# Kernel tuning notes

Measured on AMD Instinct MI355X. Metric: run time of the kernel, lower is better.

The kernel has to match this reference:

```python
import jax, jax.numpy as jnp
import numpy as np

EMB = 768
HEADS = 12
HEAD_DIM = EMB // HEADS
FF = 4 * EMB
EPS = 1e-5


def setup_inputs() -> dict:
    key = jax.random.key(0)
    ks = jax.random.split(key, 12)
    s = 0.02
    return {
        "x": jax.random.normal(ks[0], (4, 2048, EMB), dtype=jnp.float32),
        "ln1_scale": jnp.ones((EMB,), jnp.float32),
        "ln1_shift": jnp.zeros((EMB,), jnp.float32),
        # weights stored [in, out] (transpose of torch Linear layout)
        "wq": jax.random.normal(ks[1], (EMB, EMB), jnp.float32) * s,
        "wk": jax.random.normal(ks[2], (EMB, EMB), jnp.float32) * s,
        "wv": jax.random.normal(ks[3], (EMB, EMB), jnp.float32) * s,
        "wo": jax.random.normal(ks[4], (EMB, EMB), jnp.float32) * s,
        "bo": jnp.zeros((EMB,), jnp.float32),
        "ln2_scale": jnp.ones((EMB,), jnp.float32),
        "ln2_shift": jnp.zeros((EMB,), jnp.float32),
        "w1": jax.random.normal(ks[5], (EMB, FF), jnp.float32) * s,
        "b1": jnp.zeros((FF,), jnp.float32),
        "w2": jax.random.normal(ks[6], (FF, EMB), jnp.float32) * s,
        "b2": jnp.zeros((EMB,), jnp.float32),
    }


def _layernorm(x, scale, shift):
    mean = jnp.mean(x, axis=-1, keepdims=True)
    var = jnp.mean(jnp.square(x - mean), axis=-1, keepdims=True)  # unbiased=False
    return scale * (x - mean) / jnp.sqrt(var + EPS) + shift


def _gelu_tanh(x):
    c = jnp.sqrt(jnp.float32(2.0 / np.pi))
    return 0.5 * x * (1.0 + jnp.tanh(c * (x + 0.044715 * x * x * x)))


def _attention(x, wq, wk, wv, wo, bo):
    b, s, _ = x.shape
    q = (x @ wq).reshape(b, s, HEADS, HEAD_DIM).transpose(0, 2, 1, 3)
    k = (x @ wk).reshape(b, s, HEADS, HEAD_DIM).transpose(0, 2, 1, 3)
    v = (x @ wv).reshape(b, s, HEADS, HEAD_DIM).transpose(0, 2, 1, 3)
    scores = jnp.einsum("bhqd,bhkd->bhqk", q, k)  # [B,H,S,S]
    causal = jnp.tril(jnp.ones((s, s), dtype=bool))
    scores = jnp.where(causal, scores, -jnp.inf)
    weights = jax.nn.softmax(scores / jnp.sqrt(jnp.float32(HEAD_DIM)), axis=-1)
    ctx = jnp.einsum("bhqk,bhkd->bhqd", weights, v)
    ctx = ctx.transpose(0, 2, 1, 3).reshape(b, s, EMB)
    return ctx @ wo + bo


def reference(x, ln1_scale, ln1_shift, wq, wk, wv, wo, bo,
              ln2_scale, ln2_shift, w1, b1, w2, b2):
    # dropout rate is 0.0 (inference) -> identity
    x = x + _attention(_layernorm(x, ln1_scale, ln1_shift), wq, wk, wv, wo, bo)
    h = _layernorm(x, ln2_scale, ln2_shift)
    h = _gelu_tanh(h @ w1 + b1) @ w2 + b2
    return x + h
```

## Files before the change

kernel.cpp:

```cpp
#include <hip/hip_runtime.h>
#include <stdint.h>

#define EMB 768
#define SEQ 2048
#define BATCH 4
#define NHEADS 12
#define HDIM 64
#define FFDIM 3072
#define NTOK (BATCH*SEQ)
#define LNEPS 1e-5f
#define QSCALE 0.1803368801111137f

typedef __attribute__((ext_vector_type(8))) short bf16x8;
typedef __attribute__((ext_vector_type(4))) float f32x4;

__device__ __forceinline__ uint16_t f2bf(float f){
  union { float f; uint32_t u; } v; v.f = f;
  uint32_t r = v.u + 0x7fffu + ((v.u >> 16) & 1u);
  return (uint16_t)(r >> 16);
}
__device__ __forceinline__ uint32_t pk_rhu(float lo, float hi){
  union { float f; uint32_t u; } a, b; a.f = lo; b.f = hi;
  return __builtin_amdgcn_perm(b.u + 0x8000u, a.u + 0x8000u, 0x07060302u);
}

typedef __attribute__((address_space(3))) uint32_t lds32_t;
typedef __attribute__((address_space(1))) const uint32_t glb32_t;
__device__ __forceinline__ void gload16(const void* g, void* l){
  __builtin_amdgcn_global_load_lds((glb32_t*)(uintptr_t)g,
                                   (lds32_t*)(uintptr_t)l, 16, 0, 0);
}

struct TPtrs { const float* src[6]; uint16_t* dst[6]; };
__global__ __launch_bounds__(256) void transpose_all(TPtrs tp){
  int idx = blockIdx.x;
  int which, bx, by, K, N;
  if (idx < 2304){ which = idx/576; int l = idx - which*576; bx = l%24; by = l/24; K = 768;  N = 768;  }
  else if (idx < 4608){ which = 4; int l = idx-2304; bx = l%96; by = l/96; K = 768;  N = 3072; }
  else { which = 5; int l = idx-4608; bx = l%24; by = l/24; K = 3072; N = 768;  }
  const float* w = tp.src[which];
  uint16_t* wt   = tp.dst[which];
  __shared__ uint16_t tile[32][33];
  int n0 = bx*32, k0 = by*32;
  #pragma unroll
  for (int i=0;i<4;i++){
    int k = threadIdx.y + i*8;
    tile[k][threadIdx.x] = f2bf(w[(size_t)(k0+k)*N + n0 + threadIdx.x]);
  }
  __syncthreads();
  #pragma unroll
  for (int i=0;i<4;i++){
    int n = threadIdx.y + i*8;
    wt[(size_t)(n0+n)*K + k0 + threadIdx.x] = tile[threadIdx.x][n];
  }
}

__global__ __launch_bounds__(256) void ln_kernel(const float* __restrict__ x,
    const float* __restrict__ sc, const float* __restrict__ sh,
    uint16_t* __restrict__ out)
{
  int row = blockIdx.x*4 + (threadIdx.x>>6);
  int ln = threadIdx.x & 63;
  const float4* xr = (const float4*)(x + (size_t)row*EMB);
  float4 v0 = xr[ln], v1 = xr[64+ln], v2 = xr[128+ln];
  float s  = v0.x+v0.y+v0.z+v0.w + v1.x+v1.y+v1.z+v1.w + v2.x+v2.y+v2.z+v2.w;
  float s2 = v0.x*v0.x+v0.y*v0.y+v0.z*v0.z+v0.w*v0.w
           + v1.x*v1.x+v1.y*v1.y+v1.z*v1.z+v1.w*v1.w
           + v2.x*v2.x+v2.y*v2.y+v2.z*v2.z+v2.w*v2.w;
  #pragma unroll
  for (int off=1;off<64;off<<=1){ s += __shfl_xor(s,off); s2 += __shfl_xor(s2,off); }
  float mean = s*(1.f/768.f);
  float var  = s2*(1.f/768.f) - mean*mean;
  float rstd = rsqrtf(var + LNEPS);
  uint16_t* orow = out + (size_t)row*EMB;
  float4 vv[3] = {v0,v1,v2};
  #pragma unroll
  for (int i=0;i<3;i++){
    int c = (i*64+ln)*4;
    ushort4 o4;
    o4.x = f2bf((vv[i].x-mean)*rstd*sc[c+0] + sh[c+0]);
    o4.y = f2bf((vv[i].y-mean)*rstd*sc[c+1] + sh[c+1]);
    o4.z = f2bf((vv[i].z-mean)*rstd*sc[c+2] + sh[c+2]);
    o4.w = f2bf((vv[i].w-mean)*rstd*sc[c+3] + sh[c+3]);
    *(ushort4*)(orow + c) = o4;
  }
}

template<int MODE, int TM>
__global__ __launch_bounds__(256) void gemm_bt(const uint16_t* __restrict__ A,
    const uint16_t* __restrict__ Bt0,
    const float* __restrict__ bias,
    const float* __restrict__ resid,
    void* __restrict__ outp,
    uint16_t* __restrict__ vt_out,
    int N, int K, long bt_zstride, long out_zstride)
{
  constexpr int MI = TM/32;
  __shared__ __align__(16) uint16_t As[2][TM][32];
  __shared__ __align__(16) uint16_t Bs[2][128][32];
  const uint16_t* Bt = Bt0 + (size_t)blockIdx.z * bt_zstride;
  int tid = threadIdx.x;
  int wave = tid>>6, ln = tid&63, lane16 = ln&15, quad = ln>>4;
  int m0 = blockIdx.x*TM, n0 = blockIdx.y*128;
  int wm = (wave>>1)*(MI*16), wn = (wave&1)*64;
  f32x4 zf = {0.f,0.f,0.f,0.f};
  f32x4 acc[MI][4];
  #pragma unroll
  for (int i=0;i<MI;i++)
    #pragma unroll
    for (int j=0;j<4;j++) acc[i][j]=zf;
  int ar = tid>>2;
  int ac = (tid&3)*8;
  const uint16_t* Arow0 = A  + (size_t)(m0+ar)*K    + ac;
  const uint16_t* Arow1 = A  + (size_t)(m0+ar+64)*K + ac;
  const uint16_t* Brow0 = Bt + (size_t)(n0+ar)*K    + ac;
  const uint16_t* Brow1 = Bt + (size_t)(n0+ar+64)*K + ac;

  auto stage = [&](int buf, int k0){
    char* lA = (char*)&As[buf][0][0] + wave*1024;
    char* lB = (char*)&Bs[buf][0][0] + wave*1024;
    gload16(Arow0 + k0, lA);
    if (TM==128) gload16(Arow1 + k0, lA + 4096);
    gload16(Brow0 + k0, lB);
    gload16(Brow1 + k0, lB + 4096);
  };

  int niter = K>>5;
  stage(0, 0);
  for (int s=0; s<niter; s++){
    __syncthreads();
    if (s+1 < niter) stage((s+1)&1, (s+1)<<5);
    int buf = s&1;
    bf16x8 af[MI], bfr[4];
    #pragma unroll
    for (int mi=0;mi<MI;mi++) af[mi]  = *(const bf16x8*)&As[buf][wm+mi*16+lane16][quad*8];
    #pragma unroll
    for (int ni=0;ni<4;ni++)  bfr[ni] = *(const bf16x8*)&Bs[buf][wn+ni*16+lane16][quad*8];
    #pragma unroll
    for (int mi=0;mi<MI;mi++)
      #pragma unroll
      for (int ni=0;ni<4;ni++)
        acc[mi][ni] = __builtin_amdgcn_mfma_f32_16x16x32_bf16(af[mi], bfr[ni], acc[mi][ni], 0,0,0);
  }
  if (MODE==0 && blockIdx.z==2){
    #pragma unroll
    for (int mi=0;mi<MI;mi++){
      int mrow0 = m0 + wm + mi*16 + quad*4;
      int bb = mrow0 >> 11, s = mrow0 & 2047;
      #pragma unroll
      for (int ni=0;ni<4;ni++){
        int ncol = n0 + wn + ni*16 + lane16;
        int hh = ncol >> 6, dd = ncol & 63;
        ushort4 o4 = { f2bf(acc[mi][ni][0]), f2bf(acc[mi][ni][1]),
                       f2bf(acc[mi][ni][2]), f2bf(acc[mi][ni][3]) };
        *(ushort4*)(vt_out + ((size_t)((bb*NHEADS+hh)*HDIM + dd))*SEQ + s) = o4;
      }
    }
    return;
  }
  float oscale = (MODE==0 && blockIdx.z==0) ? QSCALE : 1.0f;
  #pragma unroll
  for (int mi=0;mi<MI;mi++){
    #pragma unroll
    for (int r=0;r<4;r++){
      int mrow = m0 + wm + mi*16 + quad*4 + r;
      #pragma unroll
      for (int ni=0;ni<4;ni++){
        int ncol = n0 + wn + ni*16 + lane16;
        float vv = acc[mi][ni][r];
        size_t idx = (size_t)mrow*N + ncol;
        if (MODE==0){
          ((uint16_t*)outp)[(size_t)blockIdx.z*out_zstride + idx] = f2bf(vv*oscale);
        } else if (MODE==1){
          ((float*)outp)[idx] = vv + bias[ncol] + resid[idx];
        } else if (MODE==2){
          float t = vv + bias[ncol];
          float u = 1.5957691216057308f*(t + 0.044715f*t*t*t);
          ((uint16_t*)outp)[idx] = f2bf(t / (1.f + __expf(-u)));
        } else {
          ((float*)outp)[idx] = vv + bias[ncol] + resid[idx];
        }
      }
    }
  }
}

__global__ __launch_bounds__(256, 3) void attn_kernel(const uint16_t* __restrict__ q,
    const uint16_t* __restrict__ k, const uint16_t* __restrict__ vt,
    uint16_t* __restrict__ ctx)
{
  __shared__ __align__(16) uint16_t Ks[2][8][64][8];
  __shared__ __align__(16) uint16_t Vs[2][8][64][8];
  const f32x4 zf = {0.f,0.f,0.f,0.f};
  int tid = threadIdx.x;
  int wave = tid>>6, ln = tid&63, l16 = ln&15, quad = ln>>4;
  int id  = blockIdx.x;
  int xcd = id & 7;
  int s_  = id >> 3;
  int p   = s_ & 15;
  int g   = xcd*6 + (s_ >> 4);
  int h   = g % NHEADS, b = g / NHEADS;
  size_t kgbase = ((size_t)(b*SEQ + ln))*EMB + h*HDIM;
  size_t vgbase = ((size_t)((b*NHEADS + h)*HDIM + ln))*SEQ;

  f32x4 o[4];
  float m_l, l_l;
  bf16x8 qf0, qf1;
  int q0w, myq;

  auto stage = [&](int buf, int kv0){
    #pragma unroll
    for (int i=0;i<2;i++){
      int c = wave + 4*i;
      gload16(k  + kgbase + (size_t)kv0*EMB + c*8, &Ks[buf][c][0][0]);
      gload16(vt + vgbase + kv0 + c*8,             &Vs[buf][c][0][0]);
    }
  };
  auto init_tile = [&](int tile){
    q0w = tile*64 + wave*16;
    myq = q0w + l16;
    const uint16_t* qrow = q + ((size_t)(b*SEQ + q0w + l16))*EMB + h*HDIM + quad*8;
    qf0 = *(const bf16x8*)(qrow);
    qf1 = *(const bf16x8*)(qrow + 32);
    o[0]=zf; o[1]=zf; o[2]=zf; o[3]=zf;
    m_l = -3.0e38f; l_l = 0.f;
  };
  auto writeout = [&](){
    float inv = 1.0f / l_l;
    uint16_t* crow = ctx + ((size_t)(b*SEQ + q0w + l16))*EMB + h*HDIM + quad*4;
    #pragma unroll
    for (int t=0; t<4; t++){
      ushort4 w4 = { f2bf(o[t][0]*inv), f2bf(o[t][1]*inv),
                     f2bf(o[t][2]*inv), f2bf(o[t][3]*inv) };
      *(ushort4*)(crow + t*16) = w4;
    }
  };
  auto compute = [&](int buf, int kv0, bool masked){
    bf16x8 kf[4][2], vf[2][4];
    #pragma unroll
    for (int f=0; f<4; f++){
      kf[f][0] = *(const bf16x8*)&Ks[buf][quad  ][f*16+l16][0];
      kf[f][1] = *(const bf16x8*)&Ks[buf][quad+4][f*16+l16][0];
    }
    #pragma unroll
    for (int t=0; t<4; t++){
      vf[0][t] = *(const bf16x8*)&Vs[buf][quad  ][t*16+l16][0];
      vf[1][t] = *(const bf16x8*)&Vs[buf][quad+4][t*16+l16][0];
    }
    f32x4 st[4];
    #pragma unroll
    for (int f=0; f<4; f++){
      st[f] = __builtin_amdgcn_mfma_f32_16x16x32_bf16(kf[f][0], qf0, zf, 0,0,0);
      st[f] = __builtin_amdgcn_mfma_f32_16x16x32_bf16(kf[f][1], qf1, st[f], 0,0,0);
    }
    if (masked){
      #pragma unroll
      for (int f=0; f<4; f++){
        int kvf = kv0 + f*16 + quad*4;
        #pragma unroll
        for (int r=0; r<4; r++)
          if (kvf + r > myq) st[f][r] = -1e30f;
      }
    }
    float cmax = -1e30f;
    #pragma unroll
    for (int f=0; f<4; f++)
      #pragma unroll
      for (int r=0; r<4; r++) cmax = fmaxf(cmax, st[f][r]);
    cmax = fmaxf(cmax, __shfl_xor(cmax,16));
    cmax = fmaxf(cmax, __shfl_xor(cmax,32));
    float mn = fmaxf(m_l, cmax);
    float alpha = __builtin_amdgcn_exp2f(m_l - mn);
    float rs = 0.f;
    #pragma unroll
    for (int f=0; f<4; f++)
      #pragma unroll
      for (int r=0; r<4; r++){
        st[f][r] = __builtin_amdgcn_exp2f(st[f][r] - mn);
        rs += st[f][r];
      }
    rs += __shfl_xor(rs,16); rs += __shfl_xor(rs,32);
    l_l = l_l*alpha + rs; m_l = mn;
    #pragma unroll
    for (int t=0; t<4; t++)
      #pragma unroll
      for (int r=0; r<4; r++) o[t][r] *= alpha;
    uint32_t dw[4][2];
    #pragma unroll
    for (int f=0; f<4; f++){
      dw[f][0] = pk_rhu(st[f][0], st[f][1]);
      dw[f][1] = pk_rhu(st[f][2], st[f][3]);
    }
    union { uint32_t u[4]; bf16x8 v; } pb[2];
    #pragma unroll
    for (int g2=0; g2<2; g2++)
      #pragma unroll
      for (int j=0; j<4; j++){
        int src = 16*(2*(quad&1) + (j>>1)) + l16;
        uint32_t lo = (uint32_t)__shfl((int)dw[2*g2  ][j&1], src, 64);
        uint32_t hi = (uint32_t)__shfl((int)dw[2*g2+1][j&1], src, 64);
        pb[g2].u[j] = (quad>>1) ? hi : lo;
      }
    #pragma unroll
    for (int t=0; t<4; t++){
      o[t] = __builtin_amdgcn_mfma_f32_16x16x32_bf16(vf[0][t], pb[0].v, o[t], 0,0,0);
      o[t] = __builtin_amdgcn_mfma_f32_16x16x32_bf16(vf[1][t], pb[1].v, o[t], 0,0,0);
    }
  };

  int n0 = p + 1, ntot = 33;
  init_tile(p);
  stage(0, 0);
  for (int s=0; s<ntot; s++){
    int sl = (s < n0) ? s : s - n0;
    int kv0 = sl*64;
    __syncthreads();
    if (s+1 < ntot){
      int sn = s+1;
      int snl = (sn < n0) ? sn : sn - n0;
      stage(sn&1, snl*64);
    }
    if (s == n0){ writeout(); init_tile(31 - p); }
    bool masked = (s == n0-1) || (s == ntot-1);
    compute(s&1, kv0, masked);
  }
  writeout();
}

extern "C" void kernel_launch(void* const* d_in, const int* in_sizes, int n_in,
                              void* d_out, int out_size, void* d_ws, size_t ws_size,
                              hipStream_t stream) {
  const float* x     = (const float*)d_in[0];
  const float* ln1_s = (const float*)d_in[1];
  const float* ln1_b = (const float*)d_in[2];
  const float* wq    = (const float*)d_in[3];
  const float* wk    = (const float*)d_in[4];
  const float* wv    = (const float*)d_in[5];
  const float* wo    = (const float*)d_in[6];
  const float* bo    = (const float*)d_in[7];
  const float* ln2_s = (const float*)d_in[8];
  const float* ln2_b = (const float*)d_in[9];
  const float* w1    = (const float*)d_in[10];
  const float* b1    = (const float*)d_in[11];
  const float* w2    = (const float*)d_in[12];
  const float* b2    = (const float*)d_in[13];

  uint16_t* wqkv_t = (uint16_t*)d_ws;
  uint16_t* wo_t   = wqkv_t + 3*EMB*EMB;
  uint16_t* w1_t   = wo_t   + EMB*EMB;
  uint16_t* w2_t   = w1_t   + (size_t)FFDIM*EMB;
  uint16_t* xn     = w2_t   + (size_t)EMB*FFDIM;
  uint16_t* qkv    = xn     + (size_t)NTOK*EMB;
  uint16_t* ctx    = qkv    + (size_t)3*NTOK*EMB;
  uint16_t* hff    = qkv;
  float*    x1     = (float*)(ctx + (size_t)NTOK*EMB);
  uint16_t* vt     = (uint16_t*)(x1 + (size_t)NTOK*EMB);

  TPtrs tp;
  tp.src[0]=wq; tp.src[1]=wk; tp.src[2]=wv; tp.src[3]=wo; tp.src[4]=w1; tp.src[5]=w2;
  tp.dst[0]=wqkv_t; tp.dst[1]=wqkv_t+EMB*EMB; tp.dst[2]=wqkv_t+2*EMB*EMB;
  tp.dst[3]=wo_t; tp.dst[4]=w1_t; tp.dst[5]=w2_t;
  transpose_all<<<6912, dim3(32,8), 0, stream>>>(tp);

  ln_kernel<<<NTOK/4, 256, 0, stream>>>(x, ln1_s, ln1_b, xn);
  gemm_bt<0,128><<<dim3(NTOK/128, EMB/128, 3), 256, 0, stream>>>(
      xn, wqkv_t, nullptr, nullptr, qkv, vt, EMB, EMB,
      (long)EMB*EMB, (long)NTOK*EMB);
  attn_kernel<<<768, 256, 0, stream>>>(
      qkv, qkv + (size_t)NTOK*EMB, vt, ctx);
  gemm_bt<1,64><<<dim3(NTOK/64, EMB/128, 1), 256, 0, stream>>>(
      ctx, wo_t, bo, x, x1, nullptr, EMB, EMB, 0, 0);
  ln_kernel<<<NTOK/4, 256, 0, stream>>>(x1, ln2_s, ln2_b, xn);
  gemm_bt<2,128><<<dim3(NTOK/128, FFDIM/128, 1), 256, 0, stream>>>(
      xn, w1_t, b1, nullptr, hff, nullptr, FFDIM, EMB, 0, 0);
  gemm_bt<3,64><<<dim3(NTOK/64, EMB/128, 1), 256, 0, stream>>>(
      hff, w2_t, b2, x1, d_out, nullptr, EMB, FFDIM, 0, 0);
}
```

Before: 370.4 us.

## Launch one attention block per query tile, longest-first, instead of paired tiles

The attention kernel previously paired query tile p with tile 31-p in one block so every block did 33 KV steps. Now each block handles a single query tile, with heavy tiles scheduled first (t = 31 - r/6), the grid doubles to 1536 blocks, and launch bounds rise to 5 blocks per SIMD-occupancy target. The aim is more parallelism and occupancy, with the longest-first ordering relied on for load balance. In exchange, per-block setup and staging overhead is repeated more often, and the higher occupancy target may force register spilling.

```diff
diff --git a/kernel.cpp b/kernel.cpp
--- a/kernel.cpp
+++ b/kernel.cpp
@@ -185,7 +185,7 @@
   }
 }
 
-__global__ __launch_bounds__(256, 3) void attn_kernel(const uint16_t* __restrict__ q,
+__global__ __launch_bounds__(256, 5) void attn_kernel(const uint16_t* __restrict__ q,
     const uint16_t* __restrict__ k, const uint16_t* __restrict__ vt,
     uint16_t* __restrict__ ctx)
 {
@@ -196,9 +196,9 @@
   int wave = tid>>6, ln = tid&63, l16 = ln&15, quad = ln>>4;
   int id  = blockIdx.x;
   int xcd = id & 7;
-  int s_  = id >> 3;
-  int p   = s_ & 15;
-  int g   = xcd*6 + (s_ >> 4);
+  int r_  = id >> 3;
+  int t   = 31 - (r_ / 6);
+  int g   = xcd*6 + (r_ % 6);
   int h   = g % NHEADS, b = g / NHEADS;
   size_t kgbase = ((size_t)(b*SEQ + ln))*EMB + h*HDIM;
   size_t vgbase = ((size_t)((b*NHEADS + h)*HDIM + ln))*SEQ;
@@ -229,10 +229,10 @@
     float inv = 1.0f / l_l;
     uint16_t* crow = ctx + ((size_t)(b*SEQ + q0w + l16))*EMB + h*HDIM + quad*4;
     #pragma unroll
-    for (int t=0; t<4; t++){
-      ushort4 w4 = { f2bf(o[t][0]*inv), f2bf(o[t][1]*inv),
-                     f2bf(o[t][2]*inv), f2bf(o[t][3]*inv) };
-      *(ushort4*)(crow + t*16) = w4;
+    for (int tt=0; tt<4; tt++){
+      ushort4 w4 = { f2bf(o[tt][0]*inv), f2bf(o[tt][1]*inv),
+                     f2bf(o[tt][2]*inv), f2bf(o[tt][3]*inv) };
+      *(ushort4*)(crow + tt*16) = w4;
     }
   };
   auto compute = [&](int buf, int kv0, bool masked){
@@ -243,9 +243,9 @@
       kf[f][1] = *(const bf16x8*)&Ks[buf][quad+4][f*16+l16][0];
     }
     #pragma unroll
-    for (int t=0; t<4; t++){
-      vf[0][t] = *(const bf16x8*)&Vs[buf][quad  ][t*16+l16][0];
-      vf[1][t] = *(const bf16x8*)&Vs[buf][quad+4][t*16+l16][0];
+    for (int tt=0; tt<4; tt++){
+      vf[0][tt] = *(const bf16x8*)&Vs[buf][quad  ][tt*16+l16][0];
+      vf[1][tt] = *(const bf16x8*)&Vs[buf][quad+4][tt*16+l16][0];
     }
     f32x4 st[4];
     #pragma unroll
@@ -282,9 +282,9 @@
     rs += __shfl_xor(rs,16); rs += __shfl_xor(rs,32);
     l_l = l_l*alpha + rs; m_l = mn;
     #pragma unroll
-    for (int t=0; t<4; t++)
-      #pragma unroll
-      for (int r=0; r<4; r++) o[t][r] *= alpha;
+    for (int tt=0; tt<4; tt++)
+      #pragma unroll
+      for (int r=0; r<4; r++) o[tt][r] *= alpha;
     uint32_t dw[4][2];
     #pragma unroll
     for (int f=0; f<4; f++){
@@ -302,27 +302,18 @@
         pb[g2].u[j] = (quad>>1) ? hi : lo;
       }
     #pragma unroll
-    for (int t=0; t<4; t++){
-      o[t] = __builtin_amdgcn_mfma_f32_16x16x32_bf16(vf[0][t], pb[0].v, o[t], 0,0,0);
-      o[t] = __builtin_amdgcn_mfma_f32_16x16x32_bf16(vf[1][t], pb[1].v, o[t], 0,0,0);
-    }
-  };
-
-  int n0 = p + 1, ntot = 33;
-  init_tile(p);
+    for (int tt=0; tt<4; tt++){
+      o[tt] = __builtin_amdgcn_mfma_f32_16x16x32_bf16(vf[0][tt], pb[0].v, o[tt], 0,0,0);
+      o[tt] = __builtin_amdgcn_mfma_f32_16x16x32_bf16(vf[1][tt], pb[1].v, o[tt], 0,0,0);
+    }
+  };
+
+  init_tile(t);
   stage(0, 0);
-  for (int s=0; s<ntot; s++){
-    int sl = (s < n0) ? s : s - n0;
-    int kv0 = sl*64;
+  for (int s=0; s<=t; s++){
     __syncthreads();
-    if (s+1 < ntot){
-      int sn = s+1;
-      int snl = (sn < n0) ? sn : sn - n0;
-      stage(sn&1, snl*64);
-    }
-    if (s == n0){ writeout(); init_tile(31 - p); }
-    bool masked = (s == n0-1) || (s == ntot-1);
-    compute(s&1, kv0, masked);
+    if (s+1 <= t) stage((s+1)&1, (s+1)*64);
+    compute(s&1, s*64, s == t);
   }
   writeout();
 }
@@ -366,7 +357,7 @@
   gemm_bt<0,128><<<dim3(NTOK/128, EMB/128, 3), 256, 0, stream>>>(
       xn, wqkv_t, nullptr, nullptr, qkv, vt, EMB, EMB,
       (long)EMB*EMB, (long)NTOK*EMB);
-  attn_kernel<<<768, 256, 0, stream>>>(
+  attn_kernel<<<1536, 256, 0, stream>>>(
       qkv, qkv + (size_t)NTOK*EMB, vt, ctx);
   gemm_bt<1,64><<<dim3(NTOK/64, EMB/128, 1), 256, 0, stream>>>(
       ctx, wo_t, bo, x, x1, nullptr, EMB, EMB, 0, 0);
```

Measured after the change: 369.8 us. No clear change (-0.2%).
